# Kernel optimization log

Hardware: AMD Instinct MI355X
Metric: run time of the kernel (lower is better)

The kernel has to match this reference:

```python
import jax, jax.numpy as jnp
import numpy as np

H, W, DIM, B, K = 28, 28, 384, 64, 1
EPS = 1e-5


def setup_inputs() -> dict:
    key = jax.random.key(0)
    k1, k2, k3 = jax.random.split(key, 3)
    L = 1 + K * H * W
    x = jax.random.normal(k1, (B, L, DIM), dtype=jnp.float32)
    w_reduction = jax.random.normal(k2, (2 * DIM, 4 * DIM), dtype=jnp.float32) * 0.02
    w_convert = jax.random.normal(k3, (2 * DIM, DIM), dtype=jnp.float32) * 0.02
    ln_gamma = jnp.ones((4 * DIM,), dtype=jnp.float32)
    ln_beta = jnp.zeros((4 * DIM,), dtype=jnp.float32)
    return {"x": x, "w_reduction": w_reduction, "w_convert": w_convert,
            "ln_gamma": ln_gamma, "ln_beta": ln_beta}


def reference(x, w_reduction, w_convert, ln_gamma, ln_beta):
    Bb, L, C = x.shape
    k = (L - 1) // (H * W)
    cls_token = x[:, 0:1, :]                      # [B,1,C]
    feat = x[:, 1:, :].reshape(Bb, k, H, W, C)
    x0 = feat[:, :, 0::2, 0::2, :]                # [B,k,H/2,W/2,C]
    x1 = feat[:, :, 1::2, 0::2, :]
    x2 = feat[:, :, 0::2, 1::2, :]
    x3 = feat[:, :, 1::2, 1::2, :]
    m = jnp.concatenate([x0, x1, x2, x3], axis=-1)  # [B,k,H/2,W/2,4C]
    m = m.reshape(Bb, k, -1, 4 * C)
    # LayerNorm over last dim
    mu = jnp.mean(m, axis=-1, keepdims=True)
    var = jnp.mean(jnp.square(m - mu), axis=-1, keepdims=True)
    m = (m - mu) * jax.lax.rsqrt(var + EPS) * ln_gamma + ln_beta
    red = jnp.einsum('bknf,of->bkno', m, w_reduction).reshape(Bb, -1, 2 * C)
    cls_out = jnp.einsum('bic,oc->bio', cls_token, w_convert)  # [B,1,2C]
    return jnp.concatenate([cls_out, red], axis=1)
```

## Files before the change

kernel.cpp:

```cpp
#include <hip/hip_runtime.h>
#include <hip/hip_bf16.h>

#define DIMC 384
#define LL 785
#define FDIM 1536
#define ODIM 768
#define NPATCH 196
#define MROWS 12544
#define BATCH 64

typedef __attribute__((ext_vector_type(8))) short bf16x8;
typedef __attribute__((ext_vector_type(4))) float floatx4;
typedef __attribute__((ext_vector_type(4))) unsigned short ushort4v;

#define WS_WBF_OFF  38535168
#define WS_BIAS_OFF 40894464

#define PB_CLS   0
#define PB_NORM  192
#define PB_BIAS  976
#define PB_WBF   1168
#define PREP_BLOCKS 2320

__device__ __forceinline__ unsigned short f2bf(float f) {
  union { float f; unsigned int u; } v; v.f = f;
  unsigned int u = v.u + 0x7fffu + ((v.u >> 16) & 1u);
  return (unsigned short)(u >> 16);
}

__device__ __forceinline__ void gload_lds16(const void* g, void* l) {
  __builtin_amdgcn_global_load_lds(
      (const __attribute__((address_space(1))) unsigned int*)g,
      (__attribute__((address_space(3))) unsigned int*)l, 16, 0, 0);
}

__global__ __launch_bounds__(256) void prep_kernel(
    const float* __restrict__ x, const float* __restrict__ wred,
    const float* __restrict__ wconv, const float* __restrict__ gamma,
    const float* __restrict__ beta, unsigned short* __restrict__ anorm,
    unsigned short* __restrict__ wbf, float* __restrict__ bias,
    float* __restrict__ out) {
  const int blk = blockIdx.x;
  const int t = threadIdx.x;
  const int wv = t >> 6;
  const int lane = t & 63;

  if (blk >= PB_NORM && blk < PB_BIAS) {
    int radd[6];
#pragma unroll
    for (int c = 0; c < 6; ++c) {
      int f = lane * 4 + c * 256;
      int q = f / 384;
      int cc = f - q * 384;
      radd[c] = ((q & 1) * 28 + ((q >> 1) & 1)) * DIMC + cc;
    }
    const int wvid = (blk - PB_NORM) * 4 + wv;
    const int g0 = wvid * 4;

    unsigned bo[4];
    float4 v[4][6];
    float s[4], s2[4];
#pragma unroll
    for (int r = 0; r < 4; ++r) {
      int gw = g0 + r;
      int b = gw / NPATCH;
      int n = gw - b * NPATCH;
      int i = n / 14;
      int j = n - i * 14;
      bo[r] = (unsigned)(b * LL * DIMC + DIMC + (i * 56 + j * 2) * DIMC);
      s[r] = 0.f; s2[r] = 0.f;
#pragma unroll
      for (int c = 0; c < 6; ++c) {
        float4 vv = *reinterpret_cast<const float4*>(x + bo[r] + radd[c]);
        v[r][c] = vv;
        s[r]  += vv.x + vv.y + vv.z + vv.w;
        s2[r] += vv.x * vv.x + vv.y * vv.y + vv.z * vv.z + vv.w * vv.w;
      }
    }
#pragma unroll
    for (int o = 1; o < 64; o <<= 1) {
#pragma unroll
      for (int r = 0; r < 4; ++r) {
        s[r]  += __shfl_xor(s[r], o);
        s2[r] += __shfl_xor(s2[r], o);
      }
    }
#pragma unroll
    for (int r = 0; r < 4; ++r) {
      float mu = s[r] * (1.f / FDIM);
      float var = s2[r] * (1.f / FDIM) - mu * mu;
      float rs = rsqrtf(var + 1e-5f);
      float nmu = -mu * rs;
      unsigned short* arow = anorm + (size_t)(g0 + r) * FDIM;
#pragma unroll
      for (int c = 0; c < 6; ++c) {
        float4 vv = v[r][c];
        union { ushort4v u4; __hip_bfloat162 h[2]; } u;
        u.h[0] = __float22bfloat162_rn(
            make_float2(vv.x * rs + nmu, vv.y * rs + nmu));
        u.h[1] = __float22bfloat162_rn(
            make_float2(vv.z * rs + nmu, vv.w * rs + nmu));
        *reinterpret_cast<ushort4v*>(arow + lane * 4 + c * 256) = u.u4;
      }
    }
  } else if (blk < PB_NORM) {
    __shared__ float xs[DIMC];
    int idx = blk;
    int b = idx / 3;
    int ch = idx - b * 3;
    for (int c = t; c < DIMC; c += 256) xs[c] = x[(size_t)b * LL * DIMC + c];
    __syncthreads();
    int o = ch * 256 + t;
    const float* wr = wconv + (size_t)o * DIMC;
    float a0 = 0.f, a1 = 0.f;
#pragma unroll 4
    for (int c = 0; c < DIMC; c += 8) {
      float4 w0 = *reinterpret_cast<const float4*>(wr + c);
      float4 w1 = *reinterpret_cast<const float4*>(wr + c + 4);
      float4 p0 = *reinterpret_cast<const float4*>(&xs[c]);
      float4 p1 = *reinterpret_cast<const float4*>(&xs[c + 4]);
      a0 += w0.x * p0.x + w0.y * p0.y + w0.z * p0.z + w0.w * p0.w;
      a1 += w1.x * p1.x + w1.y * p1.y + w1.z * p1.z + w1.w * p1.w;
    }
    out[(size_t)b * 197 * ODIM + o] = a0 + a1;
  } else if (blk < PB_WBF) {
    int o = (blk - PB_BIAS) * 4 + wv;
    const float* wr = wred + (size_t)o * FDIM;
    float s = 0.f;
#pragma unroll
    for (int c = 0; c < 6; ++c) {
      int f = lane * 4 + c * 256;
      float4 w = *reinterpret_cast<const float4*>(wr + f);
      float4 be = *reinterpret_cast<const float4*>(beta + f);
      s += w.x * be.x + w.y * be.y + w.z * be.z + w.w * be.w;
    }
#pragma unroll
    for (int o2 = 32; o2 > 0; o2 >>= 1) s += __shfl_down(s, o2);
    if (lane == 0) bias[o] = s;
  } else {
    int idx4 = (blk - PB_WBF) * 256 + t;
    int e0 = idx4 * 4;
    int f = e0 % FDIM;
    float4 w = *reinterpret_cast<const float4*>(wred + e0);
    float4 g = *reinterpret_cast<const float4*>(gamma + f);
    ushort4v u;
    u.x = f2bf(w.x * g.x); u.y = f2bf(w.y * g.y);
    u.z = f2bf(w.z * g.z); u.w = f2bf(w.w * g.w);
    *reinterpret_cast<ushort4v*>(wbf + e0) = u;
  }
}

__global__ __launch_bounds__(256) void gemm_kernel(
    const unsigned short* __restrict__ anorm,
    const unsigned short* __restrict__ wbf,
    const float* __restrict__ bias, float* __restrict__ out) {
  __shared__ unsigned short As[128 * 64];
  __shared__ unsigned short Bs[128 * 64];

  const int t = threadIdx.x;

  const int NWG = (ODIM / 128) * (MROWS / 128);
  const int qq = NWG >> 3, rr = NWG & 7;
  int bid = blockIdx.x;
  int xcd = bid & 7, pos = bid >> 3;
  int wg = (xcd < rr) ? xcd * (qq + 1) + pos
                      : rr * (qq + 1) + (xcd - rr) * qq + pos;
  int my = wg / 6;
  int nx = wg - my * 6;
  const int mBase = my * 128;
  const int nBase = nx * 128;

  const unsigned short* agp[4];
  const unsigned short* bgp[4];
  unsigned int ldsoff[4];
#pragma unroll
  for (int p = 0; p < 4; ++p) {
    int s = p * 256 + t;
    int r = s >> 3;
    int cs = (s & 7) ^ (r & 7);
    agp[p] = anorm + (size_t)(mBase + r) * FDIM + cs * 8;
    bgp[p] = wbf + (size_t)(nBase + r) * FDIM + cs * 8;
    ldsoff[p] = (unsigned)s * 8;
  }

  const int wv = t >> 6;
  const int lane = t & 63;
  const int ln15 = lane & 15;
  const int quad = lane >> 4;
  const int wm = wv >> 1;
  const int wn = wv & 1;

  unsigned int aoff[4][2], boff[4][2];
#pragma unroll
  for (int mt = 0; mt < 4; ++mt) {
#pragma unroll
    for (int h = 0; h < 2; ++h) {
      int rA = wm * 64 + mt * 16 + ln15;
      aoff[mt][h] = (unsigned)(rA * 64 + (((h * 4 + quad) ^ (rA & 7)) * 8));
      int rB = wn * 64 + mt * 16 + ln15;
      boff[mt][h] = (unsigned)(rB * 64 + (((h * 4 + quad) ^ (rB & 7)) * 8));
    }
  }

  floatx4 acc[4][4];
#pragma unroll
  for (int mt = 0; mt < 4; ++mt)
#pragma unroll
    for (int nt = 0; nt < 4; ++nt)
      acc[mt][nt] = floatx4{0.f, 0.f, 0.f, 0.f};

  for (int kt = 0; kt < FDIM / 64; ++kt) {
    if (kt) __syncthreads();
#pragma unroll
    for (int p = 0; p < 4; ++p) {
      gload_lds16(agp[p], &As[ldsoff[p]]);
      gload_lds16(bgp[p], &Bs[ldsoff[p]]);
      agp[p] += 64;
      bgp[p] += 64;
    }
    __syncthreads();

#pragma unroll
    for (int h = 0; h < 2; ++h) {
      bf16x8 af[4], bfr[4];
#pragma unroll
      for (int mt = 0; mt < 4; ++mt)
        af[mt] = *reinterpret_cast<const bf16x8*>(&As[aoff[mt][h]]);
#pragma unroll
      for (int nt = 0; nt < 4; ++nt)
        bfr[nt] = *reinterpret_cast<const bf16x8*>(&Bs[boff[nt][h]]);
#pragma unroll
      for (int mt = 0; mt < 4; ++mt)
#pragma unroll
        for (int nt = 0; nt < 4; ++nt)
          acc[mt][nt] = __builtin_amdgcn_mfma_f32_16x16x32_bf16(
              af[mt], bfr[nt], acc[mt][nt], 0, 0, 0);
    }
  }

  float bs[4];
#pragma unroll
  for (int nt = 0; nt < 4; ++nt)
    bs[nt] = bias[nBase + wn * 64 + nt * 16 + ln15];
#pragma unroll
  for (int mt = 0; mt < 4; ++mt) {
#pragma unroll
    for (int r = 0; r < 4; ++r) {
      int m = mBase + wm * 64 + mt * 16 + quad * 4 + r;
      int b = m / NPATCH;
      int n = m - b * NPATCH;
      float* orow = out + ((size_t)b * 197 + 1 + n) * ODIM + nBase + wn * 64;
#pragma unroll
      for (int nt = 0; nt < 4; ++nt)
        __builtin_nontemporal_store(acc[mt][nt][r] + bs[nt],
                                    &orow[nt * 16 + ln15]);
    }
  }
}

extern "C" void kernel_launch(void* const* d_in, const int* in_sizes, int n_in,
                              void* d_out, int out_size, void* d_ws, size_t ws_size,
                              hipStream_t stream) {
  const float* x     = (const float*)d_in[0];
  const float* wred  = (const float*)d_in[1];
  const float* wconv = (const float*)d_in[2];
  const float* gamma = (const float*)d_in[3];
  const float* beta  = (const float*)d_in[4];
  float* out = (float*)d_out;

  unsigned short* anorm = (unsigned short*)d_ws;
  unsigned short* wbf   = (unsigned short*)((char*)d_ws + WS_WBF_OFF);
  float* bias           = (float*)((char*)d_ws + WS_BIAS_OFF);

  prep_kernel<<<dim3(PREP_BLOCKS), 256, 0, stream>>>(x, wred, wconv, gamma,
                                                     beta, anorm, wbf, bias,
                                                     out);
  gemm_kernel<<<dim3((ODIM / 128) * (MROWS / 128)), 256, 0, stream>>>(
      anorm, wbf, bias, out);
}
```

Before: 180.4 us.

## Fold LayerNorm into GEMM epilogue and gather patches inside GEMM

Prep now casts x to bf16 in its native token layout and stores per-token sum and sum-of-squares. The GEMM gathers the four neighbouring tokens via k-tile address offsets and applies the normalization in the epilogue using precomputed W·gamma and W·beta vectors. This aims to make the prep pass a simple coalesced cast instead of a strided gather-normalize. It risks precision loss because unnormalized values are quantized to bf16 before scaling, and it adds per-iteration address math in the GEMM.

After: 174.1 us. 1.04x faster.

```diff
diff --git a/kernel.cpp b/kernel.cpp
--- a/kernel.cpp
+++ b/kernel.cpp
@@ -14,13 +14,14 @@
 typedef __attribute__((ext_vector_type(4))) unsigned short ushort4v;
 
 #define WS_WBF_OFF  38535168
-#define WS_BIAS_OFF 40894464
+#define WS_PST_OFF  40894464
+#define WS_B2_OFF   41295872
 
 #define PB_CLS   0
-#define PB_NORM  192
-#define PB_BIAS  976
-#define PB_WBF   1168
-#define PREP_BLOCKS 2320
+#define PB_CAST  192
+#define PB_BIAS  3328
+#define PB_WBF   3520
+#define PREP_BLOCKS 4672
 
 __device__ __forceinline__ unsigned short f2bf(float f) {
   union { float f; unsigned int u; } v; v.f = f;
@@ -37,73 +38,41 @@
 __global__ __launch_bounds__(256) void prep_kernel(
     const float* __restrict__ x, const float* __restrict__ wred,
     const float* __restrict__ wconv, const float* __restrict__ gamma,
-    const float* __restrict__ beta, unsigned short* __restrict__ anorm,
-    unsigned short* __restrict__ wbf, float* __restrict__ bias,
-    float* __restrict__ out) {
+    const float* __restrict__ beta, unsigned short* __restrict__ xbf,
+    unsigned short* __restrict__ wbf, float2* __restrict__ pst,
+    float2* __restrict__ bias2, float* __restrict__ out) {
   const int blk = blockIdx.x;
   const int t = threadIdx.x;
   const int wv = t >> 6;
   const int lane = t & 63;
 
-  if (blk >= PB_NORM && blk < PB_BIAS) {
-    int radd[6];
+  if (blk >= PB_CAST && blk < PB_BIAS) {
+    const int w = (blk - PB_CAST) * 4 + wv;
+    const int vid = w * 4 + (lane >> 4);
+    const int sub = lane & 15;
+    const int b = vid / 784;
+    const int ll = vid - b * 784;
+    const float* src = x + ((size_t)b * LL + 1 + ll) * DIMC;
+    unsigned short* dst = xbf + (size_t)vid * DIMC;
+    float s = 0.f, s2 = 0.f;
 #pragma unroll
     for (int c = 0; c < 6; ++c) {
-      int f = lane * 4 + c * 256;
-      int q = f / 384;
-      int cc = f - q * 384;
-      radd[c] = ((q & 1) * 28 + ((q >> 1) & 1)) * DIMC + cc;
-    }
-    const int wvid = (blk - PB_NORM) * 4 + wv;
-    const int g0 = wvid * 4;
-
-    unsigned bo[4];
-    float4 v[4][6];
-    float s[4], s2[4];
-#pragma unroll
-    for (int r = 0; r < 4; ++r) {
-      int gw = g0 + r;
-      int b = gw / NPATCH;
-      int n = gw - b * NPATCH;
-      int i = n / 14;
-      int j = n - i * 14;
-      bo[r] = (unsigned)(b * LL * DIMC + DIMC + (i * 56 + j * 2) * DIMC);
-      s[r] = 0.f; s2[r] = 0.f;
-#pragma unroll
-      for (int c = 0; c < 6; ++c) {
-        float4 vv = *reinterpret_cast<const float4*>(x + bo[r] + radd[c]);
-        v[r][c] = vv;
-        s[r]  += vv.x + vv.y + vv.z + vv.w;
-        s2[r] += vv.x * vv.x + vv.y * vv.y + vv.z * vv.z + vv.w * vv.w;
-      }
-    }
-#pragma unroll
-    for (int o = 1; o < 64; o <<= 1) {
-#pragma unroll
-      for (int r = 0; r < 4; ++r) {
-        s[r]  += __shfl_xor(s[r], o);
-        s2[r] += __shfl_xor(s2[r], o);
-      }
-    }
-#pragma unroll
-    for (int r = 0; r < 4; ++r) {
-      float mu = s[r] * (1.f / FDIM);
-      float var = s2[r] * (1.f / FDIM) - mu * mu;
-      float rs = rsqrtf(var + 1e-5f);
-      float nmu = -mu * rs;
-      unsigned short* arow = anorm + (size_t)(g0 + r) * FDIM;
-#pragma unroll
-      for (int c = 0; c < 6; ++c) {
-        float4 vv = v[r][c];
-        union { ushort4v u4; __hip_bfloat162 h[2]; } u;
-        u.h[0] = __float22bfloat162_rn(
-            make_float2(vv.x * rs + nmu, vv.y * rs + nmu));
-        u.h[1] = __float22bfloat162_rn(
-            make_float2(vv.z * rs + nmu, vv.w * rs + nmu));
-        *reinterpret_cast<ushort4v*>(arow + lane * 4 + c * 256) = u.u4;
-      }
-    }
-  } else if (blk < PB_NORM) {
+      int f = sub * 4 + c * 64;
+      float4 v = *reinterpret_cast<const float4*>(src + f);
+      s  += v.x + v.y + v.z + v.w;
+      s2 += v.x * v.x + v.y * v.y + v.z * v.z + v.w * v.w;
+      union { ushort4v u4; __hip_bfloat162 h[2]; } u;
+      u.h[0] = __float22bfloat162_rn(make_float2(v.x, v.y));
+      u.h[1] = __float22bfloat162_rn(make_float2(v.z, v.w));
+      *reinterpret_cast<ushort4v*>(dst + f) = u.u4;
+    }
+#pragma unroll
+    for (int o = 1; o < 16; o <<= 1) {
+      s  += __shfl_xor(s, o);
+      s2 += __shfl_xor(s2, o);
+    }
+    if (sub == 0) pst[vid] = make_float2(s, s2);
+  } else if (blk < PB_CAST) {
     __shared__ float xs[DIMC];
     int idx = blk;
     int b = idx / 3;
@@ -126,17 +95,22 @@
   } else if (blk < PB_WBF) {
     int o = (blk - PB_BIAS) * 4 + wv;
     const float* wr = wred + (size_t)o * FDIM;
-    float s = 0.f;
+    float sb = 0.f, sg = 0.f;
 #pragma unroll
     for (int c = 0; c < 6; ++c) {
       int f = lane * 4 + c * 256;
       float4 w = *reinterpret_cast<const float4*>(wr + f);
       float4 be = *reinterpret_cast<const float4*>(beta + f);
-      s += w.x * be.x + w.y * be.y + w.z * be.z + w.w * be.w;
-    }
-#pragma unroll
-    for (int o2 = 32; o2 > 0; o2 >>= 1) s += __shfl_down(s, o2);
-    if (lane == 0) bias[o] = s;
+      float4 ga = *reinterpret_cast<const float4*>(gamma + f);
+      sb += w.x * be.x + w.y * be.y + w.z * be.z + w.w * be.w;
+      sg += w.x * ga.x + w.y * ga.y + w.z * ga.z + w.w * ga.w;
+    }
+#pragma unroll
+    for (int o2 = 32; o2 > 0; o2 >>= 1) {
+      sb += __shfl_down(sb, o2);
+      sg += __shfl_down(sg, o2);
+    }
+    if (lane == 0) bias2[o] = make_float2(sg, sb);
   } else {
     int idx4 = (blk - PB_WBF) * 256 + t;
     int e0 = idx4 * 4;
@@ -151,11 +125,13 @@
 }
 
 __global__ __launch_bounds__(256) void gemm_kernel(
-    const unsigned short* __restrict__ anorm,
+    const unsigned short* __restrict__ xbf,
     const unsigned short* __restrict__ wbf,
-    const float* __restrict__ bias, float* __restrict__ out) {
+    const float2* __restrict__ pst, const float2* __restrict__ bias2,
+    float* __restrict__ out) {
   __shared__ unsigned short As[128 * 64];
   __shared__ unsigned short Bs[128 * 64];
+  __shared__ float2 st[128];
 
   const int t = threadIdx.x;
 
@@ -170,6 +146,25 @@
   const int mBase = my * 128;
   const int nBase = nx * 128;
 
+  if (t < 128) {
+    int m = mBase + t;
+    int b = m / NPATCH;
+    int n = m - b * NPATCH;
+    int i = n / 14;
+    int j = n - i * 14;
+    int base = b * 784 + i * 56 + j * 2;
+    float2 p0 = pst[base];
+    float2 p1 = pst[base + 28];
+    float2 p2 = pst[base + 1];
+    float2 p3 = pst[base + 29];
+    float s = p0.x + p1.x + p2.x + p3.x;
+    float s2 = p0.y + p1.y + p2.y + p3.y;
+    float mu = s * (1.f / FDIM);
+    float var = s2 * (1.f / FDIM) - mu * mu;
+    float rs = rsqrtf(var + 1e-5f);
+    st[t] = make_float2(rs, -mu * rs);
+  }
+
   const unsigned short* agp[4];
   const unsigned short* bgp[4];
   unsigned int ldsoff[4];
@@ -178,7 +173,12 @@
     int s = p * 256 + t;
     int r = s >> 3;
     int cs = (s & 7) ^ (r & 7);
-    agp[p] = anorm + (size_t)(mBase + r) * FDIM + cs * 8;
+    int m = mBase + r;
+    int b = m / NPATCH;
+    int n = m - b * NPATCH;
+    int i = n / 14;
+    int j = n - i * 14;
+    agp[p] = xbf + ((size_t)b * 784 + i * 56 + j * 2) * DIMC + cs * 8;
     bgp[p] = wbf + (size_t)(nBase + r) * FDIM + cs * 8;
     ldsoff[p] = (unsigned)s * 8;
   }
@@ -210,12 +210,14 @@
       acc[mt][nt] = floatx4{0.f, 0.f, 0.f, 0.f};
 
   for (int kt = 0; kt < FDIM / 64; ++kt) {
+    int q = kt / 6;
+    int kk = kt - q * 6;
+    int ao = ((q & 1) * 28 + ((q >> 1) & 1)) * DIMC + kk * 64;
     if (kt) __syncthreads();
 #pragma unroll
     for (int p = 0; p < 4; ++p) {
-      gload_lds16(agp[p], &As[ldsoff[p]]);
+      gload_lds16(agp[p] + ao, &As[ldsoff[p]]);
       gload_lds16(bgp[p], &Bs[ldsoff[p]]);
-      agp[p] += 64;
       bgp[p] += 64;
     }
     __syncthreads();
@@ -238,22 +240,26 @@
     }
   }
 
-  float bs[4];
+  float2 gb[4];
 #pragma unroll
   for (int nt = 0; nt < 4; ++nt)
-    bs[nt] = bias[nBase + wn * 64 + nt * 16 + ln15];
+    gb[nt] = bias2[nBase + wn * 64 + nt * 16 + ln15];
 #pragma unroll
   for (int mt = 0; mt < 4; ++mt) {
 #pragma unroll
     for (int r = 0; r < 4; ++r) {
-      int m = mBase + wm * 64 + mt * 16 + quad * 4 + r;
+      int rloc = wm * 64 + mt * 16 + quad * 4 + r;
+      float2 sn = st[rloc];
+      int m = mBase + rloc;
       int b = m / NPATCH;
       int n = m - b * NPATCH;
       float* orow = out + ((size_t)b * 197 + 1 + n) * ODIM + nBase + wn * 64;
 #pragma unroll
-      for (int nt = 0; nt < 4; ++nt)
-        __builtin_nontemporal_store(acc[mt][nt][r] + bs[nt],
-                                    &orow[nt * 16 + ln15]);
+      for (int nt = 0; nt < 4; ++nt) {
+        float val = fmaf(acc[mt][nt][r], sn.x,
+                         fmaf(sn.y, gb[nt].x, gb[nt].y));
+        __builtin_nontemporal_store(val, &orow[nt * 16 + ln15]);
+      }
     }
   }
 }
@@ -268,13 +274,14 @@
   const float* beta  = (const float*)d_in[4];
   float* out = (float*)d_out;
 
-  unsigned short* anorm = (unsigned short*)d_ws;
-  unsigned short* wbf   = (unsigned short*)((char*)d_ws + WS_WBF_OFF);
-  float* bias           = (float*)((char*)d_ws + WS_BIAS_OFF);
+  unsigned short* xbf = (unsigned short*)d_ws;
+  unsigned short* wbf = (unsigned short*)((char*)d_ws + WS_WBF_OFF);
+  float2* pst         = (float2*)((char*)d_ws + WS_PST_OFF);
+  float2* bias2       = (float2*)((char*)d_ws + WS_B2_OFF);
 
   prep_kernel<<<dim3(PREP_BLOCKS), 256, 0, stream>>>(x, wred, wconv, gamma,
-                                                     beta, anorm, wbf, bias,
-                                                     out);
+                                                     beta, xbf, wbf, pst,
+                                                     bias2, out);
   gemm_kernel<<<dim3((ODIM / 128) * (MROWS / 128)), 256, 0, stream>>>(
-      anorm, wbf, bias, out);
-}
+      xbf, wbf, pst, bias2, out);
+}
```
